# Kernel tuning notes

Hardware: AMD Instinct MI355X
Metric: run time of the kernel (lower is better)

The kernel has to match this reference:

```python
import jax, jax.numpy as jnp
import numpy as np

B, L, E, H = 1, 4096, 1024, 16
D = E // H
EPS = 1e-6


def setup_inputs() -> dict:
    key = jax.random.key(0)
    k1, k2, k3 = jax.random.split(key, 3)
    # fan-in scaled init to keep activations sane
    x = jax.random.normal(k1, (B, L, E), dtype=jnp.float32)
    qkv_w = jax.random.normal(k2, (E, 3 * E), dtype=jnp.float32) / np.sqrt(E)
    qkv_b = jnp.zeros((3 * E,), dtype=jnp.float32)
    out_w = jax.random.normal(k3, (E, E), dtype=jnp.float32) / np.sqrt(E)
    out_b = jnp.zeros((E,), dtype=jnp.float32)
    return {"x": x, "qkv_w": qkv_w, "qkv_b": qkv_b, "out_w": out_w, "out_b": out_b}


def reference(x, qkv_w, qkv_b, out_w, out_b):
    b, l, e = x.shape
    qkv = x @ qkv_w + qkv_b                      # (B, L, 3E)
    q, k, v = jnp.split(qkv, 3, axis=-1)
    # (B, L, E) -> (B, H, L, D)
    q = q.reshape(b, l, H, D).transpose(0, 2, 1, 3)
    k = k.reshape(b, l, H, D).transpose(0, 2, 1, 3)
    v = v.reshape(b, l, H, D).transpose(0, 2, 1, 3)
    q_prime = jax.nn.elu(q) + 1.0
    k_prime = jax.nn.elu(k) + 1.0
    # cumulative sum of per-position outer products k'_l v_l^T : (B,H,L,D,D)
    kv_prod = jnp.einsum('bhld,bhle->bhlde', k_prime, v)
    kv_cumsum = jnp.cumsum(kv_prod, axis=2)
    context = jnp.einsum('bhld,bhlde->bhle', q_prime, kv_cumsum)  # (B,H,L,D)
    k_cumsum = jnp.cumsum(k_prime, axis=2)                        # (B,H,L,D)
    norm = jnp.einsum('bhld,bhld->bhl', q_prime, k_cumsum)        # (B,H,L)
    output = context / (norm[..., None] + EPS)
    output = output.transpose(0, 2, 1, 3).reshape(b, l, e)
    return output @ out_w + out_b
```

## Files before the change

### kernel.cpp

```cpp
#include <hip/hip_runtime.h>
#include <cstddef>
#include <cstdint>

#define L_SEQ 4096
#define EMB   1024
#define NH    16
#define HD    64
#define N3    3072
#define CHUNK 64
#define NCHUNK 64
#define EPS 1e-6f

typedef __attribute__((ext_vector_type(8))) short   bf16x8;
typedef __attribute__((ext_vector_type(4))) short   bf16x4;
typedef __attribute__((ext_vector_type(4))) float   floatx4;

#define AS1 __attribute__((address_space(1)))
#define AS3 __attribute__((address_space(3)))

__device__ __forceinline__ void gload_lds16(const void* g, void* l) {
    __builtin_amdgcn_global_load_lds((AS1 const unsigned int*)g,
                                     (AS3 unsigned int*)l, 16, 0, 0);
}

__device__ __forceinline__ short f2bf(float f) {
    union { float f; unsigned u; } a; a.f = f;
    unsigned r = a.u + 0x7fffu + ((a.u >> 16) & 1u);
    return (short)(r >> 16);
}
__device__ __forceinline__ float bf2f(short s) {
    union { unsigned u; float f; } a; a.u = ((unsigned)(unsigned short)s) << 16;
    return a.f;
}

__device__ __forceinline__ void transpose_tile(const float* __restrict__ W,
                                               short* __restrict__ WT,
                                               int K, int N, int bx, int by,
                                               float (*t)[65], int tid)
{
    const int r  = tid >> 4;
    const int c4 = (tid & 15) << 2;
#pragma unroll
    for (int s = 0; s < 4; ++s) {
        const int k = r + s * 16;
        const floatx4 v = *(const floatx4*)&W[(size_t)(by * 64 + k) * N + bx * 64 + c4];
        t[k][c4 + 0] = v[0]; t[k][c4 + 1] = v[1];
        t[k][c4 + 2] = v[2]; t[k][c4 + 3] = v[3];
    }
    __syncthreads();
#pragma unroll
    for (int s = 0; s < 4; ++s) {
        const int n = r + s * 16;
        bf16x4 o;
        o[0] = f2bf(t[c4 + 0][n]); o[1] = f2bf(t[c4 + 1][n]);
        o[2] = f2bf(t[c4 + 2][n]); o[3] = f2bf(t[c4 + 3][n]);
        *(bf16x4*)&WT[(size_t)(bx * 64 + n) * K + by * 64 + c4] = o;
    }
}

__global__ __launch_bounds__(256)
void prep(const float* __restrict__ x, short* __restrict__ xb,
          const float* __restrict__ qkv_w, short* __restrict__ qwt,
          const float* __restrict__ out_w, short* __restrict__ owt)
{
    __shared__ float t[64][65];
    const int b = blockIdx.x;
    const int tid = threadIdx.x;
    if (b < 2048) {
        const int i = b * 256 + tid;
        const floatx4 a = *(const floatx4*)(x + (size_t)i * 8);
        const floatx4 c = *(const floatx4*)(x + (size_t)i * 8 + 4);
        bf16x8 o;
        o[0] = f2bf(a[0]); o[1] = f2bf(a[1]); o[2] = f2bf(a[2]); o[3] = f2bf(a[3]);
        o[4] = f2bf(c[0]); o[5] = f2bf(c[1]); o[6] = f2bf(c[2]); o[7] = f2bf(c[3]);
        *(bf16x8*)(xb + (size_t)i * 8) = o;
    } else if (b < 2048 + 768) {
        const int u = b - 2048;
        transpose_tile(qkv_w, qwt, EMB, N3, u % 48, u / 48, t, tid);
    } else {
        const int u = b - 2816;
        transpose_tile(out_w, owt, EMB, EMB, u & 15, u >> 4, t, tid);
    }
}

#define CST 136

__global__ __launch_bounds__(256)
void mfma_gemm_qkv(const short* __restrict__ A, const short* __restrict__ BT,
                   const float* __restrict__ bias,
                   short* __restrict__ OQ, short* __restrict__ OK,
                   short* __restrict__ OV, int N, int K)
{
    __shared__ __align__(16) short smem[128 * CST];
    short* pan[4] = { smem, smem + 4096, smem + 8192, smem + 12288 };
    const int tid  = threadIdx.x;
    const int lane = tid & 63;
    const int wave = tid >> 6;
    const int wm = (wave >> 1) * 64;
    const int wn = (wave & 1) * 64;
    const int bx = blockIdx.x;
    const int by = blockIdx.y;
    const int frow = lane & 15;
    const int quad = lane >> 4;
    const int fko  = quad << 3;

    const short* Ab = A  + (size_t)(by * 128) * K;
    const short* Bb = BT + (size_t)(bx * 128) * K;

    floatx4 acc[4][4] = {};

    for (int k0 = 0; k0 < K; k0 += 64) {
#pragma unroll
        for (int p = 0; p < 2; ++p) {
            const int kp = k0 + p * 32;
#pragma unroll
            for (int q = 0; q < 2; ++q) {
                const int ia = q * 256 + tid;
                const int row = ia >> 2;
                const int kc  = (ia & 3) << 3;
                gload_lds16(Ab + (size_t)row * K + kp + kc, &pan[p * 2 + 0][ia << 3]);
                gload_lds16(Bb + (size_t)row * K + kp + kc, &pan[p * 2 + 1][ia << 3]);
            }
        }
        __syncthreads();
#pragma unroll
        for (int p = 0; p < 2; ++p) {
            bf16x8 af[4], bfv[4];
#pragma unroll
            for (int mi = 0; mi < 4; ++mi)
                af[mi] = *(const bf16x8*)&pan[p * 2 + 0][(wm + mi * 16 + frow) * 32 + fko];
#pragma unroll
            for (int ni = 0; ni < 4; ++ni)
                bfv[ni] = *(const bf16x8*)&pan[p * 2 + 1][(wn + ni * 16 + frow) * 32 + fko];
#pragma unroll
            for (int mi = 0; mi < 4; ++mi)
#pragma unroll
                for (int ni = 0; ni < 4; ++ni)
                    acc[mi][ni] = __builtin_amdgcn_mfma_f32_16x16x32_bf16(
                        af[mi], bfv[ni], acc[mi][ni], 0, 0, 0);
        }
        __syncthreads();
    }

    const int rq = quad << 2;
#pragma unroll
    for (int ni = 0; ni < 4; ++ni) {
        const int n = bx * 128 + wn + ni * 16 + frow;
        const float bv = bias[n];
        const bool do_elu = (n >> 10) < 2;
#pragma unroll
        for (int mi = 0; mi < 4; ++mi)
#pragma unroll
            for (int r = 0; r < 4; ++r) {
                float v = acc[mi][ni][r] + bv;
                if (do_elu) v = (v > 0.f) ? (v + 1.f) : __expf(v);
                smem[(wm + mi * 16 + rq + r) * CST + wn + ni * 16 + frow] = f2bf(v);
            }
    }
    __syncthreads();
#pragma unroll
    for (int t = 0; t < 8; ++t) {
        const int idx = t * 256 + tid;
        const int mm = idx >> 4;
        const int c8 = (idx & 15) << 3;
        const bf16x8 val = *(const bf16x8*)&smem[mm * CST + c8];
        const int n0 = bx * 128 + c8;
        const int rsel = n0 >> 10;
        const int h  = (n0 & 1023) >> 6;
        const int d  = n0 & 63;
        short* base = (rsel == 0) ? OQ : (rsel == 1 ? OK : OV);
        *(bf16x8*)&base[((size_t)(h * L_SEQ + by * 128 + mm)) * HD + d] = val;
    }
}

__global__ __launch_bounds__(256)
void mfma_gemm_out(const short* __restrict__ A, const short* __restrict__ BT,
                   const float* __restrict__ bias, float* __restrict__ OF,
                   int N, int K)
{
    __shared__ __align__(16) short smem[12288];
    short* pan[4] = { smem, smem + 2048, smem + 6144, smem + 8192 };
    const int tid  = threadIdx.x;
    const int lane = tid & 63;
    const int wave = tid >> 6;
    const int wm = (wave >> 1) * 32;
    const int wn = (wave & 1) * 64;
    const int bx = blockIdx.x;
    const int by = blockIdx.y;
    const int frow = lane & 15;
    const int quad = lane >> 4;
    const int fko  = quad << 3;

    const short* Ab = A  + (size_t)(by * 64) * K;
    const short* Bb = BT + (size_t)(bx * 128) * K;

    floatx4 acc[2][4] = {};

    for (int k0 = 0; k0 < K; k0 += 64) {
#pragma unroll
        for (int p = 0; p < 2; ++p) {
            const int kp = k0 + p * 32;
            {
                const int row = tid >> 2;
                const int kc  = (tid & 3) << 3;
                gload_lds16(Ab + (size_t)row * K + kp + kc, &pan[p * 2 + 0][tid << 3]);
            }
#pragma unroll
            for (int q = 0; q < 2; ++q) {
                const int ib = q * 256 + tid;
                const int row = ib >> 2;
                const int kc  = (ib & 3) << 3;
                gload_lds16(Bb + (size_t)row * K + kp + kc, &pan[p * 2 + 1][ib << 3]);
            }
        }
        __syncthreads();
#pragma unroll
        for (int p = 0; p < 2; ++p) {
            bf16x8 af[2], bfv[4];
#pragma unroll
            for (int mi = 0; mi < 2; ++mi)
                af[mi] = *(const bf16x8*)&pan[p * 2 + 0][(wm + mi * 16 + frow) * 32 + fko];
#pragma unroll
            for (int ni = 0; ni < 4; ++ni)
                bfv[ni] = *(const bf16x8*)&pan[p * 2 + 1][(wn + ni * 16 + frow) * 32 + fko];
#pragma unroll
            for (int mi = 0; mi < 2; ++mi)
#pragma unroll
                for (int ni = 0; ni < 4; ++ni)
                    acc[mi][ni] = __builtin_amdgcn_mfma_f32_16x16x32_bf16(
                        af[mi], bfv[ni], acc[mi][ni], 0, 0, 0);
        }
        __syncthreads();
    }

    const int rq = quad << 2;
#pragma unroll
    for (int ni = 0; ni < 4; ++ni) {
        const int n = bx * 128 + wn + ni * 16 + frow;
        const float bv = bias[n];
#pragma unroll
        for (int mi = 0; mi < 2; ++mi)
#pragma unroll
            for (int r = 0; r < 4; ++r) {
                const int m = by * 64 + wm + mi * 16 + rq + r;
                OF[(size_t)m * N + n] = acc[mi][ni][r] + bv;
            }
    }
}

__global__ __launch_bounds__(256)
void chunk_state(const short* __restrict__ Kb, const short* __restrict__ Vb,
                 short* __restrict__ ScTb, float* __restrict__ zc)
{
    __shared__ float Kc[CHUNK * HD];
    __shared__ float Vc[CHUNK * HD];
    const int c = blockIdx.x, h = blockIdx.y;
    const int tid = threadIdx.x;
    const short* Kg = Kb + ((size_t)h * L_SEQ + (size_t)c * CHUNK) * HD;
    const short* Vg = Vb + ((size_t)h * L_SEQ + (size_t)c * CHUNK) * HD;
#pragma unroll
    for (int q = 0; q < 2; ++q) {
        const int idx = q * 256 + tid;
        const bf16x8 kv = *(const bf16x8*)&Kg[idx * 8];
        const bf16x8 vv = *(const bf16x8*)&Vg[idx * 8];
#pragma unroll
        for (int j = 0; j < 8; ++j) {
            Kc[idx * 8 + j] = bf2f(kv[j]);
            Vc[idx * 8 + j] = bf2f(vv[j]);
        }
    }
    __syncthreads();
    const int e0 = (tid >> 4) << 2;
    const int d0 = (tid & 15) << 2;
    float acc[4][4] = {{0.f}};
    for (int l = 0; l < CHUNK; ++l) {
        const floatx4 ve = *(const floatx4*)&Vc[l * HD + e0];
        const floatx4 kd = *(const floatx4*)&Kc[l * HD + d0];
#pragma unroll
        for (int a = 0; a < 4; ++a)
#pragma unroll
            for (int b = 0; b < 4; ++b)
                acc[a][b] += ve[a] * kd[b];
    }
    short* Sout = ScTb + (size_t)(h * NCHUNK + c) * 4096;
#pragma unroll
    for (int a = 0; a < 4; ++a) {
        bf16x4 o;
        o[0] = f2bf(acc[a][0]); o[1] = f2bf(acc[a][1]);
        o[2] = f2bf(acc[a][2]); o[3] = f2bf(acc[a][3]);
        *(bf16x4*)&Sout[(e0 + a) * HD + d0] = o;
    }
    if (tid < HD) {
        float z = 0.f;
        for (int l = 0; l < CHUNK; ++l) z += Kc[l * HD + tid];
        zc[((size_t)(h * NCHUNK + c)) * HD + tid] = z;
    }
}

__global__ __launch_bounds__(256)
void prefix_scan(const short* __restrict__ ScTb, const float* __restrict__ zc,
                 short* __restrict__ S0b)
{
    const int g = blockIdx.x * 256 + threadIdx.x;
    const int h  = g >> 12;
    const int ed = g & 4095;
    const int e  = ed >> 6;
    const int d  = ed & 63;
    const short* src = ScTb + (size_t)h * NCHUNK * 4096 + ed;
    float run = 0.f;
    for (int cb = 0; cb < NCHUNK; cb += 8) {
        short v[8];
#pragma unroll
        for (int u = 0; u < 8; ++u) v[u] = src[(size_t)(cb + u) * 4096];
#pragma unroll
        for (int u = 0; u < 8; ++u) {
            S0b[((size_t)((h * NCHUNK + cb + u) * 65 + e)) * 64 + d] = f2bf(run);
            run += bf2f(v[u]);
        }
    }
    if (g < NH * HD) {
        const int h2 = g >> 6, d2 = g & 63;
        float rz = 0.f;
        for (int cb = 0; cb < NCHUNK; cb += 8) {
            float w[8];
#pragma unroll
            for (int u = 0; u < 8; ++u)
                w[u] = zc[((size_t)(h2 * NCHUNK + cb + u)) * HD + d2];
#pragma unroll
            for (int u = 0; u < 8; ++u) {
                S0b[((size_t)((h2 * NCHUNK + cb + u) * 65 + 64)) * 64 + d2] = f2bf(rz);
                rz += w[u];
            }
        }
    }
}

#define SP 72

__global__ __launch_bounds__(256)
void chunk_attn(const short* __restrict__ Qb, const short* __restrict__ Kb,
                const short* __restrict__ Vb, const short* __restrict__ S0b,
                short* __restrict__ attn)
{
    __shared__ __align__(16) short Vs[65 * SP];
    __shared__ __align__(16) short As[64 * SP];
    const int c = blockIdx.x, h = blockIdx.y;
    const int tid = threadIdx.x, lane = tid & 63, wave = tid >> 6;
    const size_t rb = ((size_t)h * L_SEQ + (size_t)c * CHUNK) * HD;
    const short* Qg = Qb + rb;
    const short* Kg = Kb + rb;
    const short* Vg = Vb + rb;
    const short* Sg = S0b + (size_t)(h * NCHUNK + c) * 65 * 64;

#pragma unroll
    for (int q = 0; q < 2; ++q) {
        const int idx = q * 256 + tid;
        const int row = idx >> 3, c8 = (idx & 7) << 3;
        const bf16x8 vv = *(const bf16x8*)&Vg[row * 64 + c8];
#pragma unroll
        for (int j = 0; j < 8; ++j) Vs[(c8 + j) * SP + row] = vv[j];
    }
    if (tid < 64) Vs[64 * SP + tid] = (short)0x3F80;
    __syncthreads();

    const int frow = lane & 15;
    const int quad = lane >> 4;
    const int fko  = quad << 3;
    const int wm   = wave << 4;

    const bf16x8 qf0 = *(const bf16x8*)&Qg[(wm + frow) * 64 + fko];
    const bf16x8 qf1 = *(const bf16x8*)&Qg[(wm + frow) * 64 + 32 + fko];

    floatx4 sacc[4] = {};
#pragma unroll
    for (int n = 0; n < 4; ++n) {
        const bf16x8 kf0 = *(const bf16x8*)&Kg[(n * 16 + frow) * 64 + fko];
        const bf16x8 kf1 = *(const bf16x8*)&Kg[(n * 16 + frow) * 64 + 32 + fko];
        sacc[n] = __builtin_amdgcn_mfma_f32_16x16x32_bf16(qf0, kf0, sacc[n], 0, 0, 0);
        sacc[n] = __builtin_amdgcn_mfma_f32_16x16x32_bf16(qf1, kf1, sacc[n], 0, 0, 0);
    }
#pragma unroll
    for (int n = 0; n < 4; ++n)
#pragma unroll
        for (int r = 0; r < 4; ++r) {
            const int i = wm + quad * 4 + r;
            const int j = n * 16 + frow;
            As[i * SP + j] = (j <= i) ? f2bf(sacc[n][r]) : (short)0;
        }
    const bf16x8 af0 = *(const bf16x8*)&As[(wm + frow) * SP + fko];
    const bf16x8 af1 = *(const bf16x8*)&As[(wm + frow) * SP + 32 + fko];

    floatx4 oacc[5] = {};
#pragma unroll
    for (int n = 0; n < 4; ++n) {
        const bf16x8 vf0 = *(const bf16x8*)&Vs[(n * 16 + frow) * SP + fko];
        const bf16x8 vf1 = *(const bf16x8*)&Vs[(n * 16 + frow) * SP + 32 + fko];
        oacc[n] = __builtin_amdgcn_mfma_f32_16x16x32_bf16(af0, vf0, oacc[n], 0, 0, 0);
        oacc[n] = __builtin_amdgcn_mfma_f32_16x16x32_bf16(af1, vf1, oacc[n], 0, 0, 0);
        const bf16x8 sf0 = *(const bf16x8*)&Sg[(n * 16 + frow) * 64 + fko];
        const bf16x8 sf1 = *(const bf16x8*)&Sg[(n * 16 + frow) * 64 + 32 + fko];
        oacc[n] = __builtin_amdgcn_mfma_f32_16x16x32_bf16(qf0, sf0, oacc[n], 0, 0, 0);
        oacc[n] = __builtin_amdgcn_mfma_f32_16x16x32_bf16(qf1, sf1, oacc[n], 0, 0, 0);
    }
    {
        const bf16x8 vf0 = *(const bf16x8*)&Vs[64 * SP + fko];
        const bf16x8 vf1 = *(const bf16x8*)&Vs[64 * SP + 32 + fko];
        oacc[4] = __builtin_amdgcn_mfma_f32_16x16x32_bf16(af0, vf0, oacc[4], 0, 0, 0);
        oacc[4] = __builtin_amdgcn_mfma_f32_16x16x32_bf16(af1, vf1, oacc[4], 0, 0, 0);
        const bf16x8 sf0 = *(const bf16x8*)&Sg[64 * 64 + fko];
        const bf16x8 sf1 = *(const bf16x8*)&Sg[64 * 64 + 32 + fko];
        oacc[4] = __builtin_amdgcn_mfma_f32_16x16x32_bf16(qf0, sf0, oacc[4], 0, 0, 0);
        oacc[4] = __builtin_amdgcn_mfma_f32_16x16x32_bf16(qf1, sf1, oacc[4], 0, 0, 0);
    }

#pragma unroll
    for (int r = 0; r < 4; ++r) {
        const float norm = __shfl(oacc[4][r], lane & 48) + EPS;
        const float inv = 1.f / norm;
        const int i = wm + quad * 4 + r;
#pragma unroll
        for (int n = 0; n < 4; ++n)
            As[i * SP + n * 16 + frow] = f2bf(oacc[n][r] * inv);
    }
    __syncthreads();
#pragma unroll
    for (int t = 0; t < 2; ++t) {
        const int idx = t * 256 + tid;
        const int row = idx >> 3, c8 = (idx & 7) << 3;
        *(bf16x8*)&attn[(size_t)(c * CHUNK + row) * EMB + h * HD + c8] =
            *(const bf16x8*)&As[row * SP + c8];
    }
}

extern "C" void kernel_launch(void* const* d_in, const int* in_sizes, int n_in,
                              void* d_out, int out_size, void* d_ws, size_t ws_size,
                              hipStream_t stream)
{
    const float* x     = (const float*)d_in[0];
    const float* qkv_w = (const float*)d_in[1];
    const float* qkv_b = (const float*)d_in[2];
    const float* out_w = (const float*)d_in[3];
    const float* out_b = (const float*)d_in[4];
    float* out = (float*)d_out;

    short* ws    = (short*)d_ws;
    short* Qb    = ws;
    short* Kb    = Qb + 4194304;
    short* Vb    = Kb + 4194304;
    short* xb    = Vb + 4194304;
    short* qwt   = xb + 4194304;
    short* owt   = qwt + 3145728;
    short* attnb = owt + 1048576;
    short* ScTb  = attnb + 4194304;
    short* S0b   = ScTb + 4194304;
    float* zc    = (float*)(S0b + 4259840);

    prep<<<dim3(3072), 256, 0, stream>>>(x, xb, qkv_w, qwt, out_w, owt);
    mfma_gemm_qkv<<<dim3(N3 / 128, L_SEQ / 128), 256, 0, stream>>>(
        xb, qwt, qkv_b, Qb, Kb, Vb, N3, EMB);
    chunk_state<<<dim3(NCHUNK, NH), 256, 0, stream>>>(Kb, Vb, ScTb, zc);
    prefix_scan<<<dim3((NH * 4096) / 256), 256, 0, stream>>>(ScTb, zc, S0b);
    chunk_attn<<<dim3(NCHUNK, NH), 256, 0, stream>>>(Qb, Kb, Vb, S0b, attnb);
    mfma_gemm_out<<<dim3(EMB / 128, L_SEQ / 64), 256, 0, stream>>>(
        attnb, owt, out_b, out, EMB, EMB);
}
```

Measured before the change: 167.2 us.

## Use MFMA in chunk_state and shrink output GEMM tile to 32 rows

chunk_state now stages K and V transposed in LDS as bf16 and computes the per-chunk V^T K state with MFMA instructions instead of scalar fp32 FMAs. The K column sums are also done with an MFMA against a ones vector. Separately, the output projection GEMM tile is halved from 64 to 32 rows so the grid has twice as many blocks, with an occupancy hint added. The first change cuts ALU time in a small kernel; the second trades per-block data reuse for more parallelism across CUs.

```diff
diff --git a/kernel.cpp b/kernel.cpp
--- a/kernel.cpp
+++ b/kernel.cpp
@@ -173,17 +173,17 @@
     }
 }
 
-__global__ __launch_bounds__(256)
+__global__ __launch_bounds__(256, 4)
 void mfma_gemm_out(const short* __restrict__ A, const short* __restrict__ BT,
                    const float* __restrict__ bias, float* __restrict__ OF,
                    int N, int K)
 {
-    __shared__ __align__(16) short smem[12288];
-    short* pan[4] = { smem, smem + 2048, smem + 6144, smem + 8192 };
+    __shared__ __align__(16) short smem[10240];
+    short* pan[4] = { smem, smem + 1024, smem + 5120, smem + 6144 };
     const int tid  = threadIdx.x;
     const int lane = tid & 63;
     const int wave = tid >> 6;
-    const int wm = (wave >> 1) * 32;
+    const int wm = (wave >> 1) * 16;
     const int wn = (wave & 1) * 64;
     const int bx = blockIdx.x;
     const int by = blockIdx.y;
@@ -191,16 +191,16 @@
     const int quad = lane >> 4;
     const int fko  = quad << 3;
 
-    const short* Ab = A  + (size_t)(by * 64) * K;
+    const short* Ab = A  + (size_t)(by * 32) * K;
     const short* Bb = BT + (size_t)(bx * 128) * K;
 
-    floatx4 acc[2][4] = {};
+    floatx4 acc[4] = {};
 
     for (int k0 = 0; k0 < K; k0 += 64) {
 #pragma unroll
         for (int p = 0; p < 2; ++p) {
             const int kp = k0 + p * 32;
-            {
+            if (tid < 128) {
                 const int row = tid >> 2;
                 const int kc  = (tid & 3) << 3;
                 gload_lds16(Ab + (size_t)row * K + kp + kc, &pan[p * 2 + 0][tid << 3]);
@@ -216,19 +216,12 @@
         __syncthreads();
 #pragma unroll
         for (int p = 0; p < 2; ++p) {
-            bf16x8 af[2], bfv[4];
-#pragma unroll
-            for (int mi = 0; mi < 2; ++mi)
-                af[mi] = *(const bf16x8*)&pan[p * 2 + 0][(wm + mi * 16 + frow) * 32 + fko];
-#pragma unroll
-            for (int ni = 0; ni < 4; ++ni)
-                bfv[ni] = *(const bf16x8*)&pan[p * 2 + 1][(wn + ni * 16 + frow) * 32 + fko];
-#pragma unroll
-            for (int mi = 0; mi < 2; ++mi)
-#pragma unroll
-                for (int ni = 0; ni < 4; ++ni)
-                    acc[mi][ni] = __builtin_amdgcn_mfma_f32_16x16x32_bf16(
-                        af[mi], bfv[ni], acc[mi][ni], 0, 0, 0);
+            const bf16x8 af = *(const bf16x8*)&pan[p * 2 + 0][(wm + frow) * 32 + fko];
+#pragma unroll
+            for (int ni = 0; ni < 4; ++ni) {
+                const bf16x8 bfv = *(const bf16x8*)&pan[p * 2 + 1][(wn + ni * 16 + frow) * 32 + fko];
+                acc[ni] = __builtin_amdgcn_mfma_f32_16x16x32_bf16(af, bfv, acc[ni], 0, 0, 0);
+            }
         }
         __syncthreads();
     }
@@ -239,61 +232,83 @@
         const int n = bx * 128 + wn + ni * 16 + frow;
         const float bv = bias[n];
 #pragma unroll
-        for (int mi = 0; mi < 2; ++mi)
-#pragma unroll
-            for (int r = 0; r < 4; ++r) {
-                const int m = by * 64 + wm + mi * 16 + rq + r;
-                OF[(size_t)m * N + n] = acc[mi][ni][r] + bv;
-            }
-    }
-}
-
-__global__ __launch_bounds__(256)
+        for (int r = 0; r < 4; ++r) {
+            const int m = by * 32 + wm + rq + r;
+            OF[(size_t)m * N + n] = acc[ni][r] + bv;
+        }
+    }
+}
+
+#define SP 72
+
+__global__ __launch_bounds__(256, 4)
 void chunk_state(const short* __restrict__ Kb, const short* __restrict__ Vb,
                  short* __restrict__ ScTb, float* __restrict__ zc)
 {
-    __shared__ float Kc[CHUNK * HD];
-    __shared__ float Vc[CHUNK * HD];
+    __shared__ __align__(16) short Vt[64 * SP];
+    __shared__ __align__(16) short Kt[64 * SP];
     const int c = blockIdx.x, h = blockIdx.y;
-    const int tid = threadIdx.x;
+    const int tid = threadIdx.x, lane = tid & 63, wave = tid >> 6;
+    const int frow = lane & 15;
+    const int quad = lane >> 4;
+    const int fko  = quad << 3;
+    const int wm   = wave << 4;
     const short* Kg = Kb + ((size_t)h * L_SEQ + (size_t)c * CHUNK) * HD;
     const short* Vg = Vb + ((size_t)h * L_SEQ + (size_t)c * CHUNK) * HD;
+
 #pragma unroll
     for (int q = 0; q < 2; ++q) {
         const int idx = q * 256 + tid;
-        const bf16x8 kv = *(const bf16x8*)&Kg[idx * 8];
-        const bf16x8 vv = *(const bf16x8*)&Vg[idx * 8];
+        const int l = idx >> 3, c8 = (idx & 7) << 3;
+        const bf16x8 vv = *(const bf16x8*)&Vg[l * 64 + c8];
+        const bf16x8 kk = *(const bf16x8*)&Kg[l * 64 + c8];
 #pragma unroll
         for (int j = 0; j < 8; ++j) {
-            Kc[idx * 8 + j] = bf2f(kv[j]);
-            Vc[idx * 8 + j] = bf2f(vv[j]);
+            Vt[(c8 + j) * SP + l] = vv[j];
+            Kt[(c8 + j) * SP + l] = kk[j];
         }
     }
     __syncthreads();
-    const int e0 = (tid >> 4) << 2;
-    const int d0 = (tid & 15) << 2;
-    float acc[4][4] = {{0.f}};
-    for (int l = 0; l < CHUNK; ++l) {
-        const floatx4 ve = *(const floatx4*)&Vc[l * HD + e0];
-        const floatx4 kd = *(const floatx4*)&Kc[l * HD + d0];
-#pragma unroll
-        for (int a = 0; a < 4; ++a)
-#pragma unroll
-            for (int b = 0; b < 4; ++b)
-                acc[a][b] += ve[a] * kd[b];
-    }
+
+    const bf16x8 af0 = *(const bf16x8*)&Vt[(wm + frow) * SP + fko];
+    const bf16x8 af1 = *(const bf16x8*)&Vt[(wm + frow) * SP + 32 + fko];
+
+    floatx4 acc[4] = {};
+#pragma unroll
+    for (int n = 0; n < 4; ++n) {
+        const bf16x8 kf0 = *(const bf16x8*)&Kt[(n * 16 + frow) * SP + fko];
+        const bf16x8 kf1 = *(const bf16x8*)&Kt[(n * 16 + frow) * SP + 32 + fko];
+        acc[n] = __builtin_amdgcn_mfma_f32_16x16x32_bf16(af0, kf0, acc[n], 0, 0, 0);
+        acc[n] = __builtin_amdgcn_mfma_f32_16x16x32_bf16(af1, kf1, acc[n], 0, 0, 0);
+    }
+
     short* Sout = ScTb + (size_t)(h * NCHUNK + c) * 4096;
 #pragma unroll
-    for (int a = 0; a < 4; ++a) {
-        bf16x4 o;
-        o[0] = f2bf(acc[a][0]); o[1] = f2bf(acc[a][1]);
-        o[2] = f2bf(acc[a][2]); o[3] = f2bf(acc[a][3]);
-        *(bf16x4*)&Sout[(e0 + a) * HD + d0] = o;
-    }
-    if (tid < HD) {
-        float z = 0.f;
-        for (int l = 0; l < CHUNK; ++l) z += Kc[l * HD + tid];
-        zc[((size_t)(h * NCHUNK + c)) * HD + tid] = z;
+    for (int n = 0; n < 4; ++n)
+#pragma unroll
+        for (int r = 0; r < 4; ++r) {
+            const int e = wm + quad * 4 + r;
+            const int d = n * 16 + frow;
+            Sout[e * 64 + d] = f2bf(acc[n][r]);
+        }
+
+    if (wave == 0) {
+        bf16x8 ones;
+#pragma unroll
+        for (int j = 0; j < 8; ++j) ones[j] = (short)0x3F80;
+        floatx4 zacc[4] = {};
+#pragma unroll
+        for (int n = 0; n < 4; ++n) {
+            const bf16x8 kf0 = *(const bf16x8*)&Kt[(n * 16 + frow) * SP + fko];
+            const bf16x8 kf1 = *(const bf16x8*)&Kt[(n * 16 + frow) * SP + 32 + fko];
+            zacc[n] = __builtin_amdgcn_mfma_f32_16x16x32_bf16(ones, kf0, zacc[n], 0, 0, 0);
+            zacc[n] = __builtin_amdgcn_mfma_f32_16x16x32_bf16(ones, kf1, zacc[n], 0, 0, 0);
+        }
+        if (quad == 0) {
+#pragma unroll
+            for (int n = 0; n < 4; ++n)
+                zc[(size_t)(h * NCHUNK + c) * 64 + n * 16 + frow] = zacc[n][0];
+        }
     }
 }
 
@@ -335,8 +350,6 @@
     }
 }
 
-#define SP 72
-
 __global__ __launch_bounds__(256)
 void chunk_attn(const short* __restrict__ Qb, const short* __restrict__ Kb,
                 const short* __restrict__ Vb, const short* __restrict__ S0b,
@@ -412,7 +425,6 @@
         oacc[4] = __builtin_amdgcn_mfma_f32_16x16x32_bf16(qf0, sf0, oacc[4], 0, 0, 0);
         oacc[4] = __builtin_amdgcn_mfma_f32_16x16x32_bf16(qf1, sf1, oacc[4], 0, 0, 0);
     }
-
 #pragma unroll
     for (int r = 0; r < 4; ++r) {
         const float norm = __shfl(oacc[4][r], lane & 48) + EPS;
@@ -461,6 +473,6 @@
     chunk_state<<<dim3(NCHUNK, NH), 256, 0, stream>>>(Kb, Vb, ScTb, zc);
     prefix_scan<<<dim3((NH * 4096) / 256), 256, 0, stream>>>(ScTb, zc, S0b);
     chunk_attn<<<dim3(NCHUNK, NH), 256, 0, stream>>>(Qb, Kb, Vb, S0b, attnb);
-    mfma_gemm_out<<<dim3(EMB / 128, L_SEQ / 64), 256, 0, stream>>>(
+    mfma_gemm_out<<<dim3(EMB / 128, L_SEQ / 32), 256, 0, stream>>>(
         attnb, owt, out_b, out, EMB, EMB);
 }
```

Result: slower. 172.5 us (+3.1%).
